# Optimization experiments

Measured on AMD Instinct MI355X. Metric: run time of the kernel, lower is better.

The kernel has to match this reference:

```python
import jax, jax.numpy as jnp
import numpy as np

B, N, C, H = 2, 2048, 1024, 16
D = C // H  # head dim = 64
SCALE = 1.0 / (C ** 0.5)  # note: source scales by 1/sqrt(dim), not 1/sqrt(head_dim)


def setup_inputs() -> dict:
    key = jax.random.key(0)
    k1, k2, k3 = jax.random.split(key, 3)
    x = jax.random.normal(k1, (B, N, C), dtype=jnp.float32)
    w_qkv = jax.random.normal(k2, (3 * C, C), dtype=jnp.float32) * (1.0 / np.sqrt(C))
    w_proj = jax.random.normal(k3, (C, C), dtype=jnp.float32) * (1.0 / np.sqrt(C))
    b_proj = jnp.zeros((C,), dtype=jnp.float32)
    return {"x": x, "w_qkv": w_qkv, "w_proj": w_proj, "b_proj": b_proj}


def reference(x, w_qkv, w_proj, b_proj):
    Bb, Nn, Cc = x.shape
    # qkv projection (torch Linear: x @ W.T), then split into q,k,v heads
    qkv = jnp.einsum('bnc,dc->bnd', x, w_qkv)           # [B,N,3C]
    qkv = qkv.reshape(Bb, Nn, 3, H, D)
    q = qkv[:, :, 0].transpose(0, 2, 1, 3)              # [B,H,N,D]
    k = qkv[:, :, 1].transpose(0, 2, 1, 3)
    v = qkv[:, :, 2].transpose(0, 2, 1, 3)
    attn = jnp.einsum('bhnd,bhmd->bhnm', q, k) * SCALE  # [B,H,N,N]
    attn = jax.nn.softmax(attn, axis=-1)
    out = jnp.einsum('bhnm,bhmd->bhnd', attn, v)        # [B,H,N,D]
    out = out.transpose(0, 2, 1, 3).reshape(Bb, Nn, Cc)
    out = jnp.einsum('bnc,dc->bnd', out, w_proj) + b_proj
    return (out, attn)
```

## Files before the change

kernel.cpp:

```cpp
#include <hip/hip_runtime.h>

typedef __attribute__((ext_vector_type(8))) short short8;
typedef __attribute__((ext_vector_type(4))) float f32x4;
typedef __attribute__((ext_vector_type(16))) float f32x16;
typedef __attribute__((ext_vector_type(4))) unsigned int u32x4;

#define B_ 2
#define N_ 2048
#define C_ 1024
#define H_ 16
#define SCALE_ 0.03125f

__device__ inline unsigned short f2bf(float f) {
    unsigned int u = __float_as_uint(f);
    return (unsigned short)((u + 0x7fffu + ((u >> 16) & 1u)) >> 16);
}

__device__ inline f32x4 mfma16(short8 a, short8 b, f32x4 c) {
    return __builtin_amdgcn_mfma_f32_16x16x32_bf16(a, b, c, 0, 0, 0);
}
__device__ inline f32x16 mfma32(short8 a, short8 b, f32x16 c) {
    return __builtin_amdgcn_mfma_f32_32x32x16_bf16(a, b, c, 0, 0, 0);
}

#define GLOAD_LDS16(g, l) __builtin_amdgcn_global_load_lds( \
    (const __attribute__((address_space(1))) void*)(g),     \
    (__attribute__((address_space(3))) void*)(l), 16, 0, 0)

#define CVTPK(d, x, y) asm("v_cvt_pk_bf16_f32 %0, %1, %2" : "=v"(d) : "v"(x), "v"(y))
#define PLSWAP(a, b) asm volatile("v_permlane32_swap_b32 %0, %1" : "+v"(a), "+v"(b))

__global__ void cvt_all(const float* __restrict__ x, const float* __restrict__ wq,
                        const float* __restrict__ wp, unsigned short* __restrict__ xb,
                        unsigned short* __restrict__ wqb, unsigned short* __restrict__ wpb) {
    int i = blockIdx.x * blockDim.x + threadIdx.x;
    const int n1 = 4096 * 1024 / 4, n2 = 3072 * 1024 / 4;
    const float* src; unsigned short* dst; int j;
    if (i < n1)            { src = x;  dst = xb;  j = i; }
    else if (i < n1 + n2)  { src = wq; dst = wqb; j = i - n1; }
    else                   { src = wp; dst = wpb; j = i - n1 - n2; }
    float4 v = *(const float4*)(src + (size_t)j * 4);
    ushort4 o;
    o.x = f2bf(v.x); o.y = f2bf(v.y); o.z = f2bf(v.z); o.w = f2bf(v.w);
    *(ushort4*)(dst + (size_t)j * 4) = o;
}

template<int BF16_OUT, int BM>
__global__ __launch_bounds__(256, 3)
void gemm_bt(const unsigned short* __restrict__ A, const unsigned short* __restrict__ Bm,
             unsigned short* __restrict__ Cb, float* __restrict__ Cf,
             const float* __restrict__ bias, int M, int N, int K,
             int xcd_cols, int bxr) {
    constexpr int AI = BM / 32;
    __shared__ unsigned short lA[BM * 64];
    __shared__ unsigned short lB[128 * 64];
    const int tid = threadIdx.x;
    const int lane = tid & 63, wave = tid >> 6;
    const int lm = lane & 15, g = lane >> 4;
    const int flat = blockIdx.x, per = gridDim.x >> 3;
    const int xcd = flat & 7, fl = flat >> 3;
    const int rpr = per / bxr;
    const int by = (xcd / xcd_cols) * rpr + fl / bxr;
    const int bx = (xcd % xcd_cols) * bxr + fl % bxr;
    const int m0 = by * BM, n0 = bx * 128;
    const int wr = wave >> 1, wc = wave & 1;

    f32x4 acc[AI][4];
    f32x4 zero = {0.f, 0.f, 0.f, 0.f};
#pragma unroll
    for (int i = 0; i < AI; ++i)
#pragma unroll
        for (int j = 0; j < 4; ++j) acc[i][j] = zero;

    const int sRow = lane >> 3;
    const int sCol = (lane & 7) * 8;

    for (int k0 = 0; k0 < K; k0 += 64) {
#pragma unroll
        for (int t = 0; t < AI; ++t) {
            int inst = wave * AI + t;
            int r = inst * 8 + sRow;
            GLOAD_LDS16(A + (size_t)(m0 + r) * K + k0 + sCol, lA + inst * 512);
        }
#pragma unroll
        for (int t = 0; t < 4; ++t) {
            int inst = wave * 4 + t;
            int r = inst * 8 + sRow;
            GLOAD_LDS16(Bm + (size_t)(n0 + r) * K + k0 + sCol, lB + inst * 512);
        }
        __syncthreads();
#pragma unroll
        for (int kk = 0; kk < 2; ++kk) {
            short8 af[AI], bfv[4];
#pragma unroll
            for (int i = 0; i < AI; ++i)
                af[i] = *(const short8*)&lA[(wr * (BM / 2) + i * 16 + lm) * 64 + kk * 32 + g * 8];
#pragma unroll
            for (int j = 0; j < 4; ++j)
                bfv[j] = *(const short8*)&lB[(wc * 64 + j * 16 + lm) * 64 + kk * 32 + g * 8];
#pragma unroll
            for (int i = 0; i < AI; ++i)
#pragma unroll
                for (int j = 0; j < 4; ++j)
                    acc[i][j] = mfma16(af[i], bfv[j], acc[i][j]);
        }
        __syncthreads();
    }
#pragma unroll
    for (int i = 0; i < AI; ++i) {
#pragma unroll
        for (int j = 0; j < 4; ++j) {
#pragma unroll
            for (int r = 0; r < 4; ++r) {
                int m = m0 + wr * (BM / 2) + i * 16 + g * 4 + r;
                int n = n0 + wc * 64 + j * 16 + lm;
                float v = acc[i][j][r];
                if (BF16_OUT)
                    Cb[(size_t)m * N + n] = f2bf(v);
                else
                    Cf[(size_t)m * N + n] = v + bias[n];
            }
        }
    }
}

__device__ inline void stage_k256(const unsigned short* kbase, unsigned short* buf, int tid) {
    const int wave = tid >> 6, lane = tid & 63;
#pragma unroll
    for (int i = 0; i < 2; ++i) {
        int c = i * 256 + wave * 64 + lane;
        int row = c >> 3, j = c & 7;
        GLOAD_LDS16(kbase + (size_t)row * 3072 + ((j ^ (row & 7)) << 3),
                    buf + (i * 256 + wave * 64) * 8);
    }
}
__device__ inline void stage_k128(const unsigned short* kbase, unsigned short* buf, int tid) {
    const int wave = tid >> 6, lane = tid & 63;
#pragma unroll
    for (int i = 0; i < 4; ++i) {
        int c = i * 128 + wave * 64 + lane;
        int row = c >> 3, j = c & 7;
        GLOAD_LDS16(kbase + (size_t)row * 3072 + ((j ^ (row & 7)) << 3),
                    buf + (i * 128 + wave * 64) * 8);
    }
}

__global__ __launch_bounds__(128, 2)
void attn_sums(const unsigned short* __restrict__ qkv, float* __restrict__ rinv_out) {
    __shared__ unsigned short kt[2 * 4096];
    const int tid = threadIdx.x, lane = tid & 63, wave = tid >> 6;
    const int l31 = lane & 31, h5 = lane >> 5, l7 = lane & 7;
    const int flat = blockIdx.x;
    const int work = ((flat & 7) << 7) | (flat >> 3);
    const int q0 = (work & 31) * 64, h = (work >> 5) & 15, b = work >> 9;
    const unsigned short* qkvB = qkv + (size_t)b * N_ * 3072;
    const unsigned short* kh = qkvB + 1024 + h * 64;

    const unsigned short* qrow = qkvB + (size_t)(q0 + wave * 32 + l31) * 3072 + h * 64;
    short8 aq[4];
#pragma unroll
    for (int ks = 0; ks < 4; ++ks) aq[ks] = *(const short8*)(qrow + ks * 16 + h5 * 8);

    float psum = 0.f;
    stage_k128(kh, kt, tid);
    __syncthreads();

    for (int kti = 0; kti < 32; ++kti) {
        const int cur = kti & 1;
        if (kti < 31) stage_k128(kh + (size_t)(kti + 1) * 196608, kt + (cur ^ 1) * 4096, tid);
        const unsigned short* ktc = kt + cur * 4096;
        f32x16 s0 = {}, s1 = {};
        __builtin_amdgcn_s_setprio(1);
#pragma unroll
        for (int ks = 0; ks < 4; ++ks) {
            int ch = ((ks * 2 + h5) ^ l7) * 8;
            short8 b0 = *(const short8*)&ktc[l31 * 64 + ch];
            short8 b1 = *(const short8*)&ktc[(32 + l31) * 64 + ch];
            s0 = mfma32(b0, aq[ks], s0);
            s1 = mfma32(b1, aq[ks], s1);
        }
        __builtin_amdgcn_s_setprio(0);
#pragma unroll
        for (int r = 0; r < 16; ++r)
            psum += __expf(s0[r] * SCALE_) + __expf(s1[r] * SCALE_);
        __syncthreads();
    }
    psum += __shfl_xor(psum, 32);
    if (h5 == 0)
        rinv_out[(size_t)(b * H_ + h) * N_ + q0 + wave * 32 + l31] = 1.0f / psum;
}

__global__ __launch_bounds__(256, 2)
void attn_write(const unsigned short* __restrict__ qkv, const float* __restrict__ rinv_in,
                float* __restrict__ attn_out, unsigned short* __restrict__ o_out) {
    __shared__ unsigned short smem[34816];
    unsigned short* kt = smem;
    unsigned short* vt = smem + 8192;
    float* pq32 = (float*)(smem + 17408);

    const int tid = threadIdx.x, lane = tid & 63, wave = tid >> 6;
    const int l31 = lane & 31, h5 = lane >> 5, l7 = lane & 7;
    const int flat = blockIdx.x;
    const int work = ((flat & 7) << 6) | (flat >> 3);
    const int q0 = (work & 15) * 128, h = (work >> 4) & 15, b = work >> 8;
    const unsigned short* qkvB = qkv + (size_t)b * N_ * 3072;
    const unsigned short* kh = qkvB + 1024 + h * 64;
    const unsigned short* vh = qkvB + 2048 + h * 64;

    const unsigned short* qrow = qkvB + (size_t)(q0 + wave * 32 + l31) * 3072 + h * 64;
    short8 aq[4];
#pragma unroll
    for (int ks = 0; ks < 4; ++ks) aq[ks] = *(const short8*)(qrow + ks * 16 + h5 * 8);

    const float rv = rinv_in[(size_t)(b * H_ + h) * N_ + q0 + wave * 32 + l31];
    float* pw = pq32 + wave * (32 * 68);

    const int rV = (tid >> 3) * 2, cV = (tid & 7) * 8;
    short8 va, vb;
#define WRITEV(buf) do { _Pragma("unroll") for (int j = 0; j < 8; ++j) { \
        int d = cV + j; int w = (rV >> 1) ^ (((d >> 3) & 7) << 2);       \
        unsigned int pk = (unsigned int)(unsigned short)va[j] |          \
                          ((unsigned int)(unsigned short)vb[j] << 16);   \
        *(unsigned int*)&vt[(buf) * 4608 + d * 72 + 2 * w] = pk; } } while (0)

    stage_k256(kh, kt, tid);
    {
        const unsigned short* sv = vh + (size_t)rV * 3072 + cV;
        va = *(const short8*)sv; vb = *(const short8*)(sv + 3072);
    }
    WRITEV(0);
    __syncthreads();

    f32x16 oa0 = {}, oa1 = {};
    float* attnB = attn_out + ((size_t)(b * H_ + h) * N_ + q0) * N_;
    float* aw = attnB + (size_t)(wave * 32) * N_;

    for (int kti = 0; kti < 32; ++kti) {
        const int cur = kti & 1;
        if (kti < 31) {
            stage_k256(kh + (size_t)(kti + 1) * 196608, kt + (cur ^ 1) * 4096, tid);
            const unsigned short* sv = vh + (size_t)(kti + 1) * 196608 + (size_t)rV * 3072 + cV;
            va = *(const short8*)sv; vb = *(const short8*)(sv + 3072);
        }
        const unsigned short* ktc = kt + cur * 4096;
        f32x16 s0 = {}, s1 = {};
        __builtin_amdgcn_s_setprio(1);
#pragma unroll
        for (int ks = 0; ks < 4; ++ks) {
            int ch = ((ks * 2 + h5) ^ l7) * 8;
            short8 b0 = *(const short8*)&ktc[l31 * 64 + ch];
            short8 b1 = *(const short8*)&ktc[(32 + l31) * 64 + ch];
            s0 = mfma32(b0, aq[ks], s0);
            s1 = mfma32(b1, aq[ks], s1);
        }
        __builtin_amdgcn_s_setprio(0);

        unsigned int pb[16];
#pragma unroll
        for (int c4 = 0; c4 < 8; ++c4) {
            const int rb = (c4 & 3) * 4;
            f32x4 pc;
            pc.x = __expf(((c4 < 4) ? s0[rb + 0] : s1[rb + 0]) * SCALE_) * rv;
            pc.y = __expf(((c4 < 4) ? s0[rb + 1] : s1[rb + 1]) * SCALE_) * rv;
            pc.z = __expf(((c4 < 4) ? s0[rb + 2] : s1[rb + 2]) * SCALE_) * rv;
            pc.w = __expf(((c4 < 4) ? s0[rb + 3] : s1[rb + 3]) * SCALE_) * rv;
            *(f32x4*)&pw[l31 * 68 + 8 * (c4 & 3) + 32 * (c4 >> 2) + 4 * h5] = pc;
            CVTPK(pb[2 * c4], pc.x, pc.y);
            CVTPK(pb[2 * c4 + 1], pc.z, pc.w);
        }
#pragma unroll
        for (int fs = 0; fs < 4; ++fs) {
            PLSWAP(pb[4 * fs + 0], pb[4 * fs + 2]);
            PLSWAP(pb[4 * fs + 1], pb[4 * fs + 3]);
        }
#pragma unroll
        for (int rr = 0; rr < 8; ++rr) {
            int row = rr * 4 + (lane >> 4);
            f32x4 rd = *(const f32x4*)&pw[row * 68 + 4 * (lane & 15)];
            __builtin_nontemporal_store(rd,
                (f32x4*)(aw + (size_t)row * N_ + kti * 64 + 4 * (lane & 15)));
        }

        asm volatile("s_waitcnt vmcnt(8) lgkmcnt(0)\n\ts_barrier" ::: "memory");
        __builtin_amdgcn_sched_barrier(0);

        __builtin_amdgcn_s_setprio(1);
#pragma unroll
        for (int ks = 0; ks < 4; ++ks) {
            short8 ap;
            {
                u32x4 t = {pb[4 * ks + 0], pb[4 * ks + 1], pb[4 * ks + 2], pb[4 * ks + 3]};
                ap = *(short8*)&t;
            }
            int wv0 = (ks * 8 + h5 * 4) ^ (((l31 >> 3) & 7) << 2);
            short8 bv0 = *(const short8*)&vt[cur * 4608 + l31 * 72 + 2 * wv0];
            int dch = 32 + l31;
            int wv1 = (ks * 8 + h5 * 4) ^ (((dch >> 3) & 7) << 2);
            short8 bv1 = *(const short8*)&vt[cur * 4608 + dch * 72 + 2 * wv1];
            oa0 = mfma32(ap, bv0, oa0);
            oa1 = mfma32(ap, bv1, oa1);
        }
        __builtin_amdgcn_s_setprio(0);

        if (kti < 31) WRITEV(cur ^ 1);
    }

#pragma unroll
    for (int r = 0; r < 16; ++r) {
        int qrw = q0 + wave * 32 + 4 * h5 + (r & 3) + 8 * (r >> 2);
        size_t ob = (size_t)(b * N_ + qrw) * C_ + h * 64 + l31;
        o_out[ob] = f2bf(oa0[r]);
        o_out[ob + 32] = f2bf(oa1[r]);
    }
#undef WRITEV
}

extern "C" void kernel_launch(void* const* d_in, const int* in_sizes, int n_in,
                              void* d_out, int out_size, void* d_ws, size_t ws_size,
                              hipStream_t stream) {
    (void)in_sizes; (void)n_in; (void)out_size; (void)ws_size;
    const float* x      = (const float*)d_in[0];
    const float* w_qkv  = (const float*)d_in[1];
    const float* w_proj = (const float*)d_in[2];
    const float* b_proj = (const float*)d_in[3];

    float* out  = (float*)d_out;
    float* attn = out + (size_t)B_ * N_ * C_;

    unsigned short* x_b     = (unsigned short*)d_ws;
    unsigned short* wqkv_b  = x_b + (size_t)4096 * 1024;
    unsigned short* wproj_b = wqkv_b + (size_t)3072 * 1024;
    unsigned short* qkv_b   = wproj_b + (size_t)1024 * 1024;
    unsigned short* o_b     = qkv_b + (size_t)4096 * 3072;
    float* rinv = (float*)x_b;

    cvt_all<<<8192, 256, 0, stream>>>(x, w_qkv, w_proj, x_b, wqkv_b, wproj_b);

    gemm_bt<1, 128><<<768, 256, 0, stream>>>(
        x_b, wqkv_b, qkv_b, nullptr, nullptr, 4096, 3072, 1024, 2, 12);

    attn_sums<<<1024, 128, 0, stream>>>(qkv_b, rinv);
    attn_write<<<512, 256, 0, stream>>>(qkv_b, rinv, attn, o_b);

    gemm_bt<0, 64><<<512, 256, 0, stream>>>(
        o_b, wproj_b, nullptr, out, b_proj, 4096, 1024, 1024, 1, 8);
}
```

Measured before the change: 235.0 us.

## Widen attn_write key tile to 128 and restage P through a smaller LDS buffer

The attention-write kernel now processes 128 keys per iteration instead of 64, halving loop trips and barriers. It stages K with a wider loader and loads four V rows per thread into a single-buffered V tile. The fp32 probability tile is written to a smaller per-wave swizzled LDS region in four 8-row slices, so stores to the attn output cover 512-byte rows. The costs are more registers (four score accumulators, 32 packed P words), an extra barrier before the V write, and a serialized, branchy LDS transpose.

```diff
diff --git a/kernel.cpp b/kernel.cpp
--- a/kernel.cpp
+++ b/kernel.cpp
@@ -124,17 +124,7 @@
     }
 }
 
-__device__ inline void stage_k256(const unsigned short* kbase, unsigned short* buf, int tid) {
-    const int wave = tid >> 6, lane = tid & 63;
-#pragma unroll
-    for (int i = 0; i < 2; ++i) {
-        int c = i * 256 + wave * 64 + lane;
-        int row = c >> 3, j = c & 7;
-        GLOAD_LDS16(kbase + (size_t)row * 3072 + ((j ^ (row & 7)) << 3),
-                    buf + (i * 256 + wave * 64) * 8);
-    }
-}
-__device__ inline void stage_k128(const unsigned short* kbase, unsigned short* buf, int tid) {
+__device__ inline void stage_k128t(const unsigned short* kbase, unsigned short* buf, int tid) {
     const int wave = tid >> 6, lane = tid & 63;
 #pragma unroll
     for (int i = 0; i < 4; ++i) {
@@ -142,6 +132,16 @@
         int row = c >> 3, j = c & 7;
         GLOAD_LDS16(kbase + (size_t)row * 3072 + ((j ^ (row & 7)) << 3),
                     buf + (i * 128 + wave * 64) * 8);
+    }
+}
+__device__ inline void stage_k256t(const unsigned short* kbase, unsigned short* buf, int tid) {
+    const int wave = tid >> 6, lane = tid & 63;
+#pragma unroll
+    for (int i = 0; i < 4; ++i) {
+        int c = i * 256 + wave * 64 + lane;
+        int row = c >> 3, j = c & 7;
+        GLOAD_LDS16(kbase + (size_t)row * 3072 + ((j ^ (row & 7)) << 3),
+                    buf + (i * 256 + wave * 64) * 8);
     }
 }
 
@@ -162,12 +162,12 @@
     for (int ks = 0; ks < 4; ++ks) aq[ks] = *(const short8*)(qrow + ks * 16 + h5 * 8);
 
     float psum = 0.f;
-    stage_k128(kh, kt, tid);
+    stage_k128t(kh, kt, tid);
     __syncthreads();
 
     for (int kti = 0; kti < 32; ++kti) {
         const int cur = kti & 1;
-        if (kti < 31) stage_k128(kh + (size_t)(kti + 1) * 196608, kt + (cur ^ 1) * 4096, tid);
+        if (kti < 31) stage_k128t(kh + (size_t)(kti + 1) * 196608, kt + (cur ^ 1) * 4096, tid);
         const unsigned short* ktc = kt + cur * 4096;
         f32x16 s0 = {}, s1 = {};
         __builtin_amdgcn_s_setprio(1);
@@ -193,10 +193,10 @@
 __global__ __launch_bounds__(256, 2)
 void attn_write(const unsigned short* __restrict__ qkv, const float* __restrict__ rinv_in,
                 float* __restrict__ attn_out, unsigned short* __restrict__ o_out) {
-    __shared__ unsigned short smem[34816];
+    __shared__ unsigned short smem[32768];
     unsigned short* kt = smem;
-    unsigned short* vt = smem + 8192;
-    float* pq32 = (float*)(smem + 17408);
+    unsigned short* vt = smem + 16384;
+    float* pw = (float*)(smem + 24576);
 
     const int tid = threadIdx.x, lane = tid & 63, wave = tid >> 6;
     const int l31 = lane & 31, h5 = lane >> 5, l7 = lane & 7;
@@ -213,96 +213,129 @@
     for (int ks = 0; ks < 4; ++ks) aq[ks] = *(const short8*)(qrow + ks * 16 + h5 * 8);
 
     const float rv = rinv_in[(size_t)(b * H_ + h) * N_ + q0 + wave * 32 + l31];
-    float* pw = pq32 + wave * (32 * 68);
 
     const int rV = (tid >> 3) * 2, cV = (tid & 7) * 8;
-    short8 va, vb;
-#define WRITEV(buf) do { _Pragma("unroll") for (int j = 0; j < 8; ++j) { \
-        int d = cV + j; int w = (rV >> 1) ^ (((d >> 3) & 7) << 2);       \
-        unsigned int pk = (unsigned int)(unsigned short)va[j] |          \
-                          ((unsigned int)(unsigned short)vb[j] << 16);   \
-        *(unsigned int*)&vt[(buf) * 4608 + d * 72 + 2 * w] = pk; } } while (0)
-
-    stage_k256(kh, kt, tid);
-    {
-        const unsigned short* sv = vh + (size_t)rV * 3072 + cV;
-        va = *(const short8*)sv; vb = *(const short8*)(sv + 3072);
-    }
-    WRITEV(0);
+    short8 va, vb, vc, vd;
+#define LOADV(base_) do { const unsigned short* sv = (base_) + (size_t)rV * 3072 + cV;   \
+        va = *(const short8*)sv; vb = *(const short8*)(sv + 3072);                       \
+        vc = *(const short8*)(sv + (size_t)64 * 3072);                                   \
+        vd = *(const short8*)(sv + (size_t)65 * 3072); } while (0)
+#define WRITEV() do { _Pragma("unroll") for (int j = 0; j < 8; ++j) {     \
+        int d = cV + j; int w = (rV >> 1) ^ (((d >> 3) & 7) << 2);        \
+        *(unsigned int*)&vt[d * 64 + 2 * w] =                             \
+            (unsigned int)(unsigned short)va[j] |                         \
+            ((unsigned int)(unsigned short)vb[j] << 16);                  \
+        *(unsigned int*)&vt[4096 + d * 64 + 2 * w] =                      \
+            (unsigned int)(unsigned short)vc[j] |                         \
+            ((unsigned int)(unsigned short)vd[j] << 16); } } while (0)
+
+    stage_k256t(kh, kt, tid);
+    LOADV(vh);
+    WRITEV();
     __syncthreads();
 
     f32x16 oa0 = {}, oa1 = {};
     float* attnB = attn_out + ((size_t)(b * H_ + h) * N_ + q0) * N_;
     float* aw = attnB + (size_t)(wave * 32) * N_;
-
-    for (int kti = 0; kti < 32; ++kti) {
+    float* pww = pw + wave * 1024;
+
+    for (int kti = 0; kti < 16; ++kti) {
         const int cur = kti & 1;
-        if (kti < 31) {
-            stage_k256(kh + (size_t)(kti + 1) * 196608, kt + (cur ^ 1) * 4096, tid);
-            const unsigned short* sv = vh + (size_t)(kti + 1) * 196608 + (size_t)rV * 3072 + cV;
-            va = *(const short8*)sv; vb = *(const short8*)(sv + 3072);
-        }
-        const unsigned short* ktc = kt + cur * 4096;
-        f32x16 s0 = {}, s1 = {};
+        if (kti > 0) {
+            asm volatile("s_waitcnt vmcnt(16) lgkmcnt(0)\n\ts_barrier" ::: "memory");
+            __builtin_amdgcn_sched_barrier(0);
+        }
+        if (kti < 15) {
+            stage_k256t(kh + (size_t)(kti + 1) * 393216, kt + (cur ^ 1) * 8192, tid);
+            LOADV(vh + (size_t)(kti + 1) * 393216);
+        }
+        const unsigned short* ktc = kt + cur * 8192;
+        f32x16 s[4];
+        s[0] = (f32x16){}; s[1] = (f32x16){}; s[2] = (f32x16){}; s[3] = (f32x16){};
         __builtin_amdgcn_s_setprio(1);
 #pragma unroll
-        for (int ks = 0; ks < 4; ++ks) {
-            int ch = ((ks * 2 + h5) ^ l7) * 8;
-            short8 b0 = *(const short8*)&ktc[l31 * 64 + ch];
-            short8 b1 = *(const short8*)&ktc[(32 + l31) * 64 + ch];
-            s0 = mfma32(b0, aq[ks], s0);
-            s1 = mfma32(b1, aq[ks], s1);
-        }
+        for (int a = 0; a < 4; ++a)
+#pragma unroll
+            for (int ks = 0; ks < 4; ++ks) {
+                short8 kf = *(const short8*)&ktc[(a * 32 + l31) * 64 + ((ks * 2 + h5) ^ l7) * 8];
+                s[a] = mfma32(kf, aq[ks], s[a]);
+            }
         __builtin_amdgcn_s_setprio(0);
 
-        unsigned int pb[16];
-#pragma unroll
-        for (int c4 = 0; c4 < 8; ++c4) {
-            const int rb = (c4 & 3) * 4;
-            f32x4 pc;
-            pc.x = __expf(((c4 < 4) ? s0[rb + 0] : s1[rb + 0]) * SCALE_) * rv;
-            pc.y = __expf(((c4 < 4) ? s0[rb + 1] : s1[rb + 1]) * SCALE_) * rv;
-            pc.z = __expf(((c4 < 4) ? s0[rb + 2] : s1[rb + 2]) * SCALE_) * rv;
-            pc.w = __expf(((c4 < 4) ? s0[rb + 3] : s1[rb + 3]) * SCALE_) * rv;
-            *(f32x4*)&pw[l31 * 68 + 8 * (c4 & 3) + 32 * (c4 >> 2) + 4 * h5] = pc;
-            CVTPK(pb[2 * c4], pc.x, pc.y);
-            CVTPK(pb[2 * c4 + 1], pc.z, pc.w);
-        }
-#pragma unroll
-        for (int fs = 0; fs < 4; ++fs) {
-            PLSWAP(pb[4 * fs + 0], pb[4 * fs + 2]);
-            PLSWAP(pb[4 * fs + 1], pb[4 * fs + 3]);
-        }
-#pragma unroll
-        for (int rr = 0; rr < 8; ++rr) {
-            int row = rr * 4 + (lane >> 4);
-            f32x4 rd = *(const f32x4*)&pw[row * 68 + 4 * (lane & 15)];
-            __builtin_nontemporal_store(rd,
-                (f32x4*)(aw + (size_t)row * N_ + kti * 64 + 4 * (lane & 15)));
-        }
-
-        asm volatile("s_waitcnt vmcnt(8) lgkmcnt(0)\n\ts_barrier" ::: "memory");
-        __builtin_amdgcn_sched_barrier(0);
+#pragma unroll
+        for (int a = 0; a < 4; ++a)
+#pragma unroll
+            for (int r = 0; r < 16; ++r)
+                s[a][r] = __expf(s[a][r] * SCALE_) * rv;
+
+#pragma unroll
+        for (int bs = 0; bs < 4; ++bs) {
+            if ((l31 >> 3) == bs) {
+                int r7 = l31 & 7;
+                float* pr = pww + r7 * 128;
+#pragma unroll
+                for (int a = 0; a < 4; ++a)
+#pragma unroll
+                    for (int j = 0; j < 4; ++j) {
+                        int col = a * 32 + 8 * j + 4 * h5;
+                        f32x4 pv = {s[a][4 * j], s[a][4 * j + 1], s[a][4 * j + 2], s[a][4 * j + 3]};
+                        *(f32x4*)&pr[col ^ (r7 << 2)] = pv;
+                    }
+            }
+#pragma unroll
+            for (int j2 = 0; j2 < 4; ++j2) {
+                int row = 8 * bs + 2 * j2 + h5;
+                int r7s = row & 7;
+                f32x4 vvv = *(const f32x4*)&pww[r7s * 128 + ((4 * l31) ^ (r7s << 2))];
+                __builtin_nontemporal_store(vvv,
+                    (f32x4*)(aw + (size_t)row * N_ + kti * 128 + 4 * l31));
+            }
+        }
+
+        unsigned int pb[32];
+#pragma unroll
+        for (int g2 = 0; g2 < 2; ++g2) {
+#pragma unroll
+            for (int c4 = 0; c4 < 8; ++c4) {
+                int rb = (c4 & 3) * 4;
+                const f32x16& sv2 = s[2 * g2 + (c4 >> 2)];
+                CVTPK(pb[16 * g2 + 2 * c4], sv2[rb], sv2[rb + 1]);
+                CVTPK(pb[16 * g2 + 2 * c4 + 1], sv2[rb + 2], sv2[rb + 3]);
+            }
+#pragma unroll
+            for (int fs = 0; fs < 4; ++fs) {
+                PLSWAP(pb[16 * g2 + 4 * fs + 0], pb[16 * g2 + 4 * fs + 2]);
+                PLSWAP(pb[16 * g2 + 4 * fs + 1], pb[16 * g2 + 4 * fs + 3]);
+            }
+        }
 
         __builtin_amdgcn_s_setprio(1);
 #pragma unroll
-        for (int ks = 0; ks < 4; ++ks) {
-            short8 ap;
-            {
-                u32x4 t = {pb[4 * ks + 0], pb[4 * ks + 1], pb[4 * ks + 2], pb[4 * ks + 3]};
-                ap = *(short8*)&t;
-            }
-            int wv0 = (ks * 8 + h5 * 4) ^ (((l31 >> 3) & 7) << 2);
-            short8 bv0 = *(const short8*)&vt[cur * 4608 + l31 * 72 + 2 * wv0];
-            int dch = 32 + l31;
-            int wv1 = (ks * 8 + h5 * 4) ^ (((dch >> 3) & 7) << 2);
-            short8 bv1 = *(const short8*)&vt[cur * 4608 + dch * 72 + 2 * wv1];
-            oa0 = mfma32(ap, bv0, oa0);
-            oa1 = mfma32(ap, bv1, oa1);
-        }
+        for (int g2 = 0; g2 < 2; ++g2)
+#pragma unroll
+            for (int ks = 0; ks < 4; ++ks) {
+                short8 ap;
+                {
+                    u32x4 t = {pb[16 * g2 + 4 * ks], pb[16 * g2 + 4 * ks + 1],
+                               pb[16 * g2 + 4 * ks + 2], pb[16 * g2 + 4 * ks + 3]};
+                    ap = *(short8*)&t;
+                }
+                int wbase = ks * 8 + h5 * 4;
+                int w0 = wbase ^ (((l31 >> 3) & 7) << 2);
+                short8 bv0 = *(const short8*)&vt[g2 * 4096 + l31 * 64 + 2 * w0];
+                int d1 = 32 + l31;
+                int w1 = wbase ^ (((d1 >> 3) & 7) << 2);
+                short8 bv1 = *(const short8*)&vt[g2 * 4096 + d1 * 64 + 2 * w1];
+                oa0 = mfma32(ap, bv0, oa0);
+                oa1 = mfma32(ap, bv1, oa1);
+            }
         __builtin_amdgcn_s_setprio(0);
 
-        if (kti < 31) WRITEV(cur ^ 1);
+        if (kti < 15) {
+            asm volatile("s_waitcnt lgkmcnt(0)\n\ts_barrier" ::: "memory");
+            __builtin_amdgcn_sched_barrier(0);
+            WRITEV();
+        }
     }
 
 #pragma unroll
@@ -313,6 +346,7 @@
         o_out[ob + 32] = f2bf(oa1[r]);
     }
 #undef WRITEV
+#undef LOADV
 }
 
 extern "C" void kernel_launch(void* const* d_in, const int* in_sizes, int n_in,
```

Result: faster. 215.9 us (-8.1%).
